# Kernel optimization log

Measured on AMD Instinct MI355X. Metric: run time of the kernel, lower is better.

The kernel has to match this reference:

```python
import jax, jax.numpy as jnp
import numpy as np

UNITS = 65
BATCH = 50
SEQ = 8192


def setup_inputs() -> dict:
    key = jax.random.key(0)
    ks = jax.random.split(key, 6)
    x = jax.random.normal(ks[0], (BATCH, SEQ, UNITS), dtype=jnp.float32)
    # Single shared LSTM cell (same cell object reused for all 3 stacked layers)
    W = jax.random.normal(ks[1], (UNITS, 4 * UNITS), dtype=jnp.float32) * 0.1
    U = jax.random.normal(ks[2], (UNITS, 4 * UNITS), dtype=jnp.float32) * 0.1
    b = jax.random.normal(ks[3], (4 * UNITS,), dtype=jnp.float32) * 0.1
    # Dense output projection 65 -> 65
    Wd = jax.random.normal(ks[4], (UNITS, UNITS), dtype=jnp.float32) * 0.1
    bd = jax.random.normal(ks[5], (UNITS,), dtype=jnp.float32) * 0.1
    return {"x": x, "W": W, "U": U, "b": b, "Wd": Wd, "bd": bd}


def _lstm_cell(x_t, h, c, W, U, b):
    # Keras LSTMCell: gates in order i, f, g(candidate), o
    z = x_t @ W + h @ U + b                      # [B, 4*units]
    i, f, g, o = jnp.split(z, 4, axis=-1)
    i = jax.nn.sigmoid(i)
    f = jax.nn.sigmoid(f)
    g = jnp.tanh(g)
    o = jax.nn.sigmoid(o)
    c_new = f * c + i * g
    h_new = o * jnp.tanh(c_new)
    return h_new, c_new


def reference(x, W, U, b, Wd, bd):
    B = x.shape[0]
    zeros = jnp.zeros((B, UNITS), dtype=x.dtype)
    init = (zeros, zeros, zeros, zeros, zeros, zeros)  # (h1,c1,h2,c2,h3,c3)

    def step(carry, x_t):
        h1, c1, h2, c2, h3, c3 = carry
        h1, c1 = _lstm_cell(x_t, h1, c1, W, U, b)  # layer 1 (shared weights)
        h2, c2 = _lstm_cell(h1, h2, c2, W, U, b)   # layer 2 (shared weights)
        h3, c3 = _lstm_cell(h2, h3, c3, W, U, b)   # layer 3 (shared weights)
        return (h1, c1, h2, c2, h3, c3), h3

    xs = jnp.swapaxes(x, 0, 1)                   # [T, B, 65]
    _, ys = jax.lax.scan(step, init, xs)         # ys: [T, B, 65]
    ys = jnp.swapaxes(ys, 0, 1)                  # [B, T, 65]
    out = ys @ Wd + bd                           # dense projection to vocab 65
    return out
```

## Files before the change

kernel.cpp:

```cpp
#include <hip/hip_runtime.h>

#define UNITS 65
#define SEQ   8192
#define BATCH 50
#define LAYER 192

typedef float v2f __attribute__((ext_vector_type(2)));

__device__ __forceinline__ float frcp(float x){ return __builtin_amdgcn_rcpf(x); }
__device__ __forceinline__ float fsigmoid(float x){ return frcp(1.0f + __expf(-x)); }
__device__ __forceinline__ float ftanh(float x){
    float e2 = __expf(2.0f * x);
    return 1.0f - 2.0f * frcp(e2 + 1.0f);
}

template<int CTRL>
__device__ __forceinline__ float dppadd(float x){
    int t = __builtin_amdgcn_update_dpp(0, __float_as_int(x), CTRL, 0xF, 0xF, true);
    return x + __int_as_float(t);
}
template<int CTRL>
__device__ __forceinline__ float dppmov(float x){
    int t = __builtin_amdgcn_update_dpp(0, __float_as_int(x), CTRL, 0xF, 0xF, true);
    return __int_as_float(t);
}
__device__ __forceinline__ float red4_all(float x){
    x = dppadd<0xB1>(x);
    x = dppadd<0x4E>(x);
    return x;
}
__device__ __forceinline__ float red16_lane15(float x){
    x = dppadd<0x111>(x);
    x = dppadd<0x112>(x);
    x = dppadd<0x114>(x);
    x = dppadd<0x118>(x);
    return x;
}
__device__ __forceinline__ void bar_lds(){
    asm volatile("s_waitcnt lgkmcnt(0)\n\ts_barrier" ::: "memory");
}
__device__ __forceinline__ float rdlane(float v, int l){
    return __int_as_float(__builtin_amdgcn_readlane(__float_as_int(v), l));
}

__device__ __forceinline__ int inpos16(int k){
    return (k < 120) ? ((k >> 3) * 12 + (k & 7)) : (180 + (k - 120));
}
__device__ __forceinline__ float wrow(const float* W, const float* U, int k, int c){
    return (k < 65) ? W[k * 260 + c] : U[(k - 65) * 260 + c];
}


#define LAYERB(aI, aF, aG, aO, CST, ...) do {                                  \
    float qI_ = red4_all(aI), qF_ = red4_all(aF);                              \
    float qG_ = red4_all(aG), qO_ = red4_all(aO);                              \
    float z_ = ((gsel == 0) ? qI_ : (gsel == 1) ? qF_ : (gsel == 2) ? qG_ : qO_); \
    z_ = dppadd<0x114>(z_);                        \
    z_ = dppadd<0x118>(z_);              \
    z_ += breg;                                                                \
    float sg_ = frcp(1.0f + __expf(-sk * z_));                                 \
    float g_  = fmaf(sk, sg_, dk);                \
    float gi_ = dppmov<0x113>(g_);                   \
    float gf_ = dppmov<0x112>(g_);                   \
    float gg_ = dppmov<0x111>(g_);                   \
    float cn_ = fmaf(gf_, CST, gi_ * gg_);                                     \
    float hn_ = g_ * ftanh(cn_);                                               \
    if (wr) { CST = cn_; __VA_ARGS__; }                                        \
} while (0)

#define STEP(L0, L1, L2, VB, NB) do {                                          \
    const float* __restrict__ vbase = (VB);                                    \
    float*       __restrict__ nbase = (NB);                                    \
          \
    float xq1 = 0.0f, ex1 = 0.0f;                                              \
    if (L0) {                                                                  \
        const int tl_ = (s + 2 < SEQ) ? (s + 2) : (SEQ - 1);                   \
        if (wr) xq1 = xrow[(size_t)tl_ * UNITS + j];                           \
        if (wave == 1 && lane == 0) ex1 = xrow[(size_t)tl_ * UNITS + 64];      \
    }                                                                          \
       \
    const float* vp0_ = vbase + k16 * 12;                                      \
    const float* vp1_ = vbase + LAYER + k16 * 12;                              \
    const float* vp2_ = vbase + 2 * LAYER + k16 * 12;                          \
    v2f aIF0={0,0},aGO0={0,0}, aIF1={0,0},aGO1={0,0}, aIF2={0,0},aGO2={0,0};   \
    _Pragma("unroll")                                                          \
    for (int q4_ = 0; q4_ < 2; ++q4_) {                                        \
        float4 f0_, f1_, f2_;                                                  \
        if (L0) f0_ = *(const float4*)(vp0_ + 4 * q4_);                        \
        if (L1) f1_ = *(const float4*)(vp1_ + 4 * q4_);                        \
        if (L2) f2_ = *(const float4*)(vp2_ + 4 * q4_);                        \
        _Pragma("unroll")                                                      \
        for (int r_ = 0; r_ < 4; ++r_) {                                       \
            const int kk = 4 * q4_ + r_;                                       \
            if (L0) { float s0_ = (&f0_.x)[r_]; v2f ss_ = {s0_, s0_};          \
                aIF0 = __builtin_elementwise_fma(ss_, wIF[kk], aIF0);          \
                aGO0 = __builtin_elementwise_fma(ss_, wGO[kk], aGO0); }        \
            if (L1) { float s1_ = (&f1_.x)[r_]; v2f ss_ = {s1_, s1_};          \
                aIF1 = __builtin_elementwise_fma(ss_, wIF[kk], aIF1);          \
                aGO1 = __builtin_elementwise_fma(ss_, wGO[kk], aGO1); }        \
            if (L2) { float s2_ = (&f2_.x)[r_]; v2f ss_ = {s2_, s2_};          \
                aIF2 = __builtin_elementwise_fma(ss_, wIF[kk], aIF2);          \
                aGO2 = __builtin_elementwise_fma(ss_, wGO[kk], aGO2); }        \
        }                                                                      \
    }                                                                          \
    {           \
        float2 t0_, t1_, t2_;                                                  \
        if (L0) t0_ = *(const float2*)(vp0_ + 8);                              \
        if (L1) t1_ = *(const float2*)(vp1_ + 8);                              \
        if (L2) t2_ = *(const float2*)(vp2_ + 8);                              \
        _Pragma("unroll")                                                      \
        for (int r_ = 0; r_ < 2; ++r_) {                                       \
            const int kk = 8 + r_;                                             \
            if (L0) { float s0_ = (&t0_.x)[r_]; v2f ss_ = {s0_, s0_};          \
                aIF0 = __builtin_elementwise_fma(ss_, wIF[kk], aIF0);          \
                aGO0 = __builtin_elementwise_fma(ss_, wGO[kk], aGO0); }        \
            if (L1) { float s1_ = (&t1_.x)[r_]; v2f ss_ = {s1_, s1_};          \
                aIF1 = __builtin_elementwise_fma(ss_, wIF[kk], aIF1);          \
                aGO1 = __builtin_elementwise_fma(ss_, wGO[kk], aGO1); }        \
            if (L2) { float s2_ = (&t2_.x)[r_]; v2f ss_ = {s2_, s2_};          \
                aIF2 = __builtin_elementwise_fma(ss_, wIF[kk], aIF2);          \
                aGO2 = __builtin_elementwise_fma(ss_, wGO[kk], aGO2); }        \
        }                                                                      \
    }                                                                          \
          \
    const bool act64_ = (wave == 1) ? (bool)(L0)                               \
                      : (wave == 2) ? (bool)(L1)                               \
                      : (wave == 3) ? (bool)(L2) : false;                      \
    float a64_ = 0.0f;                                                         \
    if (act64_) {                                                              \
        const float* vm_ = vbase + ml * LAYER;                                 \
        float4 uA_ = *(const float4*)(vm_ + p64);                              \
        float4 uB_ = *(const float4*)(vm_ + p64 + 4);                          \
        float  uex_ = (i64 < 2) ? vm_[188 + i64] : 0.0f;                       \
        a64_ = uA_.x * w64[0];                                                 \
        a64_ = fmaf(uA_.y, w64[1], a64_); a64_ = fmaf(uA_.z, w64[2], a64_);    \
        a64_ = fmaf(uA_.w, w64[3], a64_); a64_ = fmaf(uB_.x, w64[4], a64_);    \
        a64_ = fmaf(uB_.y, w64[5], a64_); a64_ = fmaf(uB_.z, w64[6], a64_);    \
        a64_ = fmaf(uB_.w, w64[7], a64_); a64_ = fmaf(uex_, w64x, a64_);       \
        a64_ = red16_lane15(a64_);                                             \
    }                                                                          \
                                            \
    if (L0) LAYERB(aIF0.x, aIF0.y, aGO0.x, aGO0.y, c1,                         \
                   nbase[ipH] = hn_; nbase[LAYER + ipI] = hn_);                \
    if (L1) LAYERB(aIF1.x, aIF1.y, aGO1.x, aGO1.y, c2,                         \
                   nbase[LAYER + ipH] = hn_; nbase[2 * LAYER + ipI] = hn_);    \
    if (L2) LAYERB(aIF2.x, aIF2.y, aGO2.x, aGO2.y, c3,                         \
                   nbase[2 * LAYER + ipH] = hn_;                               \
                   orow[(size_t)(s - 2) * UNITS + j] = hn_);                   \
    if (L0) { if (wr) { nbase[ipI] = xq0; xq0 = xq1; } }                       \
                               \
    if (act64_) {                                                              \
        float zi_ = rdlane(a64_, 15) + b64i;                                   \
        float zf_ = rdlane(a64_, 31) + b64f;                                   \
        float zg_ = rdlane(a64_, 47) + b64g;                                   \
        float zo_ = rdlane(a64_, 63) + b64o;                                   \
        float gi4_ = fsigmoid(zi_), gf4_ = fsigmoid(zf_);                      \
        float gg4_ = ftanh(zg_),    go4_ = fsigmoid(zo_);                      \
        float cn64_ = fmaf(gf4_, c64, gi4_ * gg4_);                            \
        float hn64_ = go4_ * ftanh(cn64_);                                     \
        c64 = cn64_;                                                           \
        if (lane == 0) {                                                       \
            nbase[ml * LAYER + 189] = hn64_;                     \
            if (wave <= 2) nbase[(ml + 1) * LAYER + 96] = hn64_;  \
            else orow[(size_t)(s - 2) * UNITS + 64] = hn64_;                   \
        }                                                                      \
        if (wave == 1) { if (lane == 0) nbase[96] = ex0; ex0 = ex1; }          \
    }                                                                          \
    bar_lds();                                                                 \
} while (0)

__global__ __launch_bounds__(1024, 4)
void lstm3_kernel(const float* __restrict__ x, const float* __restrict__ W,
                  const float* __restrict__ U, const float* __restrict__ b,
                  float* __restrict__ out)
{
    const int e    = blockIdx.x;
    const int tid  = threadIdx.x;
    const int wave = tid >> 6, lane = tid & 63;
    const int k16  = lane & 15, ul = lane >> 4;
    const int j    = wave * 4 + ul;
    const int gsel = k16 & 3;
    const bool wr  = (k16 == 15);

    __shared__ __attribute__((aligned(16))) float vbuf[2][3][LAYER];

    v2f wIF[10], wGO[10];
    #pragma unroll
    for (int kk = 0; kk < 10; ++kk) {
        const int  k   = 8 * k16 + kk;
        const bool val = (kk < 8) || (k16 == 15);
        wIF[kk].x = val ? wrow(W, U, k, j)       : 0.0f;
        wIF[kk].y = val ? wrow(W, U, k, 65  + j) : 0.0f;
        wGO[kk].x = val ? wrow(W, U, k, 130 + j) : 0.0f;
        wGO[kk].y = val ? wrow(W, U, k, 195 + j) : 0.0f;
    }
    const float breg = b[gsel * 65 + j];
    const float sk   = (gsel == 2) ? 2.0f : 1.0f;
    const float dk   = 1.0f - sk;

    const int i64 = lane & 15, g64 = lane >> 4;
    const int p64 = i64 * 12;
    float w64[8], w64x;
    {
        const int c64c = g64 * 65 + 64;
        #pragma unroll
        for (int r = 0; r < 8; ++r) w64[r] = wrow(W, U, 8 * i64 + r, c64c);
        w64x = (i64 < 2) ? wrow(W, U, 128 + i64, c64c) : 0.0f;
    }

    #pragma unroll
    for (int kk = 0; kk < 10; ++kk) {
        asm volatile("" : "+v"(wIF[kk]), "+v"(wGO[kk]));
    }
    #pragma unroll
    for (int r = 0; r < 8; ++r) { asm volatile("" : "+v"(w64[r])); }
    asm volatile("" : "+v"(w64x));

    const float b64i = b[64], b64f = b[129], b64g = b[194], b64o = b[259];
    const int ml = (wave >= 1 && wave <= 3) ? (wave - 1) : 0;

    float c1 = 0, c2 = 0, c3 = 0, c64 = 0;

    const float* xrow = x   + (size_t)e * SEQ * UNITS;
    float*       orow = out + (size_t)e * SEQ * UNITS;
    const int ipI = inpos16(j), ipH = inpos16(65 + j);

    for (int i = tid; i < 2 * 3 * LAYER; i += 1024) ((float*)&vbuf[0][0][0])[i] = 0.0f;
    __syncthreads();
    if (wr)  vbuf[0][0][ipI] = xrow[j];
    if (wave == 1 && lane == 0) vbuf[0][0][96] = xrow[64];
    __syncthreads();

    float xq0 = 0, ex0 = 0;
    if (wr) xq0 = xrow[UNITS + j];
    if (wave == 1 && lane == 0) ex0 = xrow[UNITS + 64];

    float* const vb0 = &vbuf[0][0][0];
    float* const vb1 = &vbuf[1][0][0];
    int s = 0;
    STEP(1, 0, 0, vb0, vb1); ++s;
    STEP(1, 1, 0, vb1, vb0); ++s;
    for (; s < SEQ - 1; ) {
        STEP(1, 1, 1, vb0, vb1); ++s;
        STEP(1, 1, 1, vb1, vb0); ++s;
    }
    STEP(0, 1, 1, vb0, vb1); ++s;
    STEP(0, 0, 1, vb1, vb0);
}

__global__ __launch_bounds__(256)
void dense_kernel(float* __restrict__ io,
                  const float* __restrict__ Wd,
                  const float* __restrict__ bd)
{
    __shared__ __attribute__((aligned(16))) float wS[65 * 68];
    __shared__ float bS[65];
    for (int i = threadIdx.x; i < 65 * 65; i += 256) {
        int r = i / 65, c = i - r * 65;
        wS[r * 68 + c] = Wd[i];
    }
    if (threadIdx.x < 65) bS[threadIdx.x] = bd[threadIdx.x];
    __syncthreads();

    const size_t row  = (size_t)blockIdx.x * 256 + threadIdx.x;
    const size_t base = row * 65;

    float r[65];
    #pragma unroll
    for (int k = 0; k < 65; ++k) r[k] = io[base + k];

    for (int ct = 0; ct < 16; ++ct) {
        const int c = ct * 4;
        float a0 = bS[c], a1 = bS[c + 1], a2 = bS[c + 2], a3 = bS[c + 3];
        #pragma unroll
        for (int k = 0; k < 65; ++k) {
            const float4 wv = *reinterpret_cast<const float4*>(&wS[k * 68 + c]);
            a0 += r[k] * wv.x;
            a1 += r[k] * wv.y;
            a2 += r[k] * wv.z;
            a3 += r[k] * wv.w;
        }
        io[base + c]     = a0;
        io[base + c + 1] = a1;
        io[base + c + 2] = a2;
        io[base + c + 3] = a3;
    }
    float a = bS[64];
    #pragma unroll
    for (int k = 0; k < 65; ++k) a += r[k] * wS[k * 68 + 64];
    io[base + 64] = a;
}

extern "C" void kernel_launch(void* const* d_in, const int* in_sizes, int n_in,
                              void* d_out, int out_size, void* d_ws, size_t ws_size,
                              hipStream_t stream)
{
    const float* x  = (const float*)d_in[0];
    const float* W  = (const float*)d_in[1];
    const float* U  = (const float*)d_in[2];
    const float* b  = (const float*)d_in[3];
    const float* Wd = (const float*)d_in[4];
    const float* bd = (const float*)d_in[5];
    float* out = (float*)d_out;

    hipLaunchKernelGGL(lstm3_kernel, dim3(BATCH), dim3(1024), 0, stream, x, W, U, b, out);
    hipLaunchKernelGGL(dense_kernel, dim3(1600), dim3(256), 0, stream, out, Wd, bd);
}
```

Measured before the change: 15.17 ms.

## Software-pipeline per-layer LDS reads, FMAs and gate math with wave-rotated layer order

Restructures each timestep so the three stacked layers are processed as a pipeline: it reads the next layer's LDS vector while finishing the FMAs and gate activations of the previous one. Each wave starts at a different layer (wave % 3), which spreads LDS bank traffic and SALU/transcendental work across waves. The unit-64 projection loads are hoisted ahead of the pipelined body, and the asm register pins on the weights are removed. Register pressure and code size grow because all three layer paths are instantiated per wave, and the three-way branch on wro adds control flow.

```diff
diff --git a/kernel.cpp b/kernel.cpp
--- a/kernel.cpp
+++ b/kernel.cpp
@@ -68,6 +68,53 @@
     if (wr) { CST = cn_; __VA_ARGS__; }                                        \
 } while (0)
 
+#define WRT_0  nbase[ipH] = hn_; nbase[LAYER + ipI] = hn_
+#define WRT_1  nbase[LAYER + ipH] = hn_; nbase[2 * LAYER + ipI] = hn_
+#define WRT_2  nbase[2 * LAYER + ipH] = hn_; orow[(size_t)(s - 2) * UNITS + j] = hn_
+
+#define RD(l, Lact) do { if (Lact) {                                           \
+    const float* vp_ = vbase + (l) * LAYER + k16 * 12;                         \
+    fA##l = *(const float4*)(vp_);                                             \
+    fB##l = *(const float4*)(vp_ + 4);                                         \
+    fT##l = *(const float2*)(vp_ + 8);                                         \
+} } while (0)
+
+#define FM(l, Lact) do { if (Lact) {                                           \
+    _Pragma("unroll")                                                          \
+    for (int r_ = 0; r_ < 4; ++r_) {                                           \
+        float s_ = (&fA##l.x)[r_]; v2f ss_ = {s_, s_};                         \
+        aIF##l = __builtin_elementwise_fma(ss_, wIF[r_], aIF##l);              \
+        aGO##l = __builtin_elementwise_fma(ss_, wGO[r_], aGO##l);              \
+    }                                                                          \
+    _Pragma("unroll")                                                          \
+    for (int r_ = 0; r_ < 4; ++r_) {                                           \
+        float s_ = (&fB##l.x)[r_]; v2f ss_ = {s_, s_};                         \
+        aIF##l = __builtin_elementwise_fma(ss_, wIF[4 + r_], aIF##l);          \
+        aGO##l = __builtin_elementwise_fma(ss_, wGO[4 + r_], aGO##l);          \
+    }                                                                          \
+    _Pragma("unroll")                                                          \
+    for (int r_ = 0; r_ < 2; ++r_) {                                           \
+        float s_ = (&fT##l.x)[r_]; v2f ss_ = {s_, s_};                         \
+        aIF##l = __builtin_elementwise_fma(ss_, wIF[8 + r_], aIF##l);          \
+        aGO##l = __builtin_elementwise_fma(ss_, wGO[8 + r_], aGO##l);          \
+    }                                                                          \
+} } while (0)
+
+#define PB0(Lact) do { if (Lact) LAYERB(aIF0.x, aIF0.y, aGO0.x, aGO0.y, c_0, WRT_0); } while (0)
+#define PB1(Lact) do { if (Lact) LAYERB(aIF1.x, aIF1.y, aGO1.x, aGO1.y, c_1, WRT_1); } while (0)
+#define PB2(Lact) do { if (Lact) LAYERB(aIF2.x, aIF2.y, aGO2.x, aGO2.y, c_2, WRT_2); } while (0)
+
+#define PIPE3(a, b, c, La, Lb, Lc) do {                                        \
+    RD(a, La); FM(a, La);                                                      \
+    RD(b, Lb);                                                                 \
+    PB##a(La);                                                                 \
+    FM(b, Lb);                                                                 \
+    RD(c, Lc);                                                                 \
+    PB##b(Lb);                                                                 \
+    FM(c, Lc);                                                                 \
+    PB##c(Lc);                                                                 \
+} while (0)
+
 #define STEP(L0, L1, L2, VB, NB) do {                                          \
     const float* __restrict__ vbase = (VB);                                    \
     float*       __restrict__ nbase = (NB);                                    \
@@ -79,77 +126,31 @@
         if (wave == 1 && lane == 0) ex1 = xrow[(size_t)tl_ * UNITS + 64];      \
     }                                                                          \
        \
-    const float* vp0_ = vbase + k16 * 12;                                      \
-    const float* vp1_ = vbase + LAYER + k16 * 12;                              \
-    const float* vp2_ = vbase + 2 * LAYER + k16 * 12;                          \
-    v2f aIF0={0,0},aGO0={0,0}, aIF1={0,0},aGO1={0,0}, aIF2={0,0},aGO2={0,0};   \
-    _Pragma("unroll")                                                          \
-    for (int q4_ = 0; q4_ < 2; ++q4_) {                                        \
-        float4 f0_, f1_, f2_;                                                  \
-        if (L0) f0_ = *(const float4*)(vp0_ + 4 * q4_);                        \
-        if (L1) f1_ = *(const float4*)(vp1_ + 4 * q4_);                        \
-        if (L2) f2_ = *(const float4*)(vp2_ + 4 * q4_);                        \
-        _Pragma("unroll")                                                      \
-        for (int r_ = 0; r_ < 4; ++r_) {                                       \
-            const int kk = 4 * q4_ + r_;                                       \
-            if (L0) { float s0_ = (&f0_.x)[r_]; v2f ss_ = {s0_, s0_};          \
-                aIF0 = __builtin_elementwise_fma(ss_, wIF[kk], aIF0);          \
-                aGO0 = __builtin_elementwise_fma(ss_, wGO[kk], aGO0); }        \
-            if (L1) { float s1_ = (&f1_.x)[r_]; v2f ss_ = {s1_, s1_};          \
-                aIF1 = __builtin_elementwise_fma(ss_, wIF[kk], aIF1);          \
-                aGO1 = __builtin_elementwise_fma(ss_, wGO[kk], aGO1); }        \
-            if (L2) { float s2_ = (&f2_.x)[r_]; v2f ss_ = {s2_, s2_};          \
-                aIF2 = __builtin_elementwise_fma(ss_, wIF[kk], aIF2);          \
-                aGO2 = __builtin_elementwise_fma(ss_, wGO[kk], aGO2); }        \
-        }                                                                      \
-    }                                                                          \
-    {           \
-        float2 t0_, t1_, t2_;                                                  \
-        if (L0) t0_ = *(const float2*)(vp0_ + 8);                              \
-        if (L1) t1_ = *(const float2*)(vp1_ + 8);                              \
-        if (L2) t2_ = *(const float2*)(vp2_ + 8);                              \
-        _Pragma("unroll")                                                      \
-        for (int r_ = 0; r_ < 2; ++r_) {                                       \
-            const int kk = 8 + r_;                                             \
-            if (L0) { float s0_ = (&t0_.x)[r_]; v2f ss_ = {s0_, s0_};          \
-                aIF0 = __builtin_elementwise_fma(ss_, wIF[kk], aIF0);          \
-                aGO0 = __builtin_elementwise_fma(ss_, wGO[kk], aGO0); }        \
-            if (L1) { float s1_ = (&t1_.x)[r_]; v2f ss_ = {s1_, s1_};          \
-                aIF1 = __builtin_elementwise_fma(ss_, wIF[kk], aIF1);          \
-                aGO1 = __builtin_elementwise_fma(ss_, wGO[kk], aGO1); }        \
-            if (L2) { float s2_ = (&t2_.x)[r_]; v2f ss_ = {s2_, s2_};          \
-                aIF2 = __builtin_elementwise_fma(ss_, wIF[kk], aIF2);          \
-                aGO2 = __builtin_elementwise_fma(ss_, wGO[kk], aGO2); }        \
-        }                                                                      \
-    }                                                                          \
-          \
     const bool act64_ = (wave == 1) ? (bool)(L0)                               \
                       : (wave == 2) ? (bool)(L1)                               \
                       : (wave == 3) ? (bool)(L2) : false;                      \
-    float a64_ = 0.0f;                                                         \
+    float4 uA_ = {0,0,0,0}, uB_ = {0,0,0,0}; float uex_ = 0.0f;                \
     if (act64_) {                                                              \
         const float* vm_ = vbase + ml * LAYER;                                 \
-        float4 uA_ = *(const float4*)(vm_ + p64);                              \
-        float4 uB_ = *(const float4*)(vm_ + p64 + 4);                          \
-        float  uex_ = (i64 < 2) ? vm_[188 + i64] : 0.0f;                       \
-        a64_ = uA_.x * w64[0];                                                 \
+        uA_ = *(const float4*)(vm_ + p64);                                     \
+        uB_ = *(const float4*)(vm_ + p64 + 4);                                 \
+        uex_ = (i64 < 2) ? vm_[188 + i64] : 0.0f;                              \
+    }                                                                          \
+    float4 fA0, fB0, fA1, fB1, fA2, fB2; float2 fT0, fT1, fT2;                 \
+    v2f aIF0={0,0},aGO0={0,0}, aIF1={0,0},aGO1={0,0}, aIF2={0,0},aGO2={0,0};   \
+           \
+    if (wro == 0)      PIPE3(0, 1, 2, L0, L1, L2);                             \
+    else if (wro == 1) PIPE3(1, 2, 0, L1, L2, L0);                             \
+    else               PIPE3(2, 0, 1, L2, L0, L1);                             \
+    if (L0) { if (wr) { nbase[ipI] = xq0; xq0 = xq1; } }                       \
+                 \
+    if (act64_) {                                                              \
+        float a64_ = uA_.x * w64[0];                                           \
         a64_ = fmaf(uA_.y, w64[1], a64_); a64_ = fmaf(uA_.z, w64[2], a64_);    \
         a64_ = fmaf(uA_.w, w64[3], a64_); a64_ = fmaf(uB_.x, w64[4], a64_);    \
         a64_ = fmaf(uB_.y, w64[5], a64_); a64_ = fmaf(uB_.z, w64[6], a64_);    \
         a64_ = fmaf(uB_.w, w64[7], a64_); a64_ = fmaf(uex_, w64x, a64_);       \
         a64_ = red16_lane15(a64_);                                             \
-    }                                                                          \
-                                            \
-    if (L0) LAYERB(aIF0.x, aIF0.y, aGO0.x, aGO0.y, c1,                         \
-                   nbase[ipH] = hn_; nbase[LAYER + ipI] = hn_);                \
-    if (L1) LAYERB(aIF1.x, aIF1.y, aGO1.x, aGO1.y, c2,                         \
-                   nbase[LAYER + ipH] = hn_; nbase[2 * LAYER + ipI] = hn_);    \
-    if (L2) LAYERB(aIF2.x, aIF2.y, aGO2.x, aGO2.y, c3,                         \
-                   nbase[2 * LAYER + ipH] = hn_;                               \
-                   orow[(size_t)(s - 2) * UNITS + j] = hn_);                   \
-    if (L0) { if (wr) { nbase[ipI] = xq0; xq0 = xq1; } }                       \
-                               \
-    if (act64_) {                                                              \
         float zi_ = rdlane(a64_, 15) + b64i;                                   \
         float zf_ = rdlane(a64_, 31) + b64f;                                   \
         float zg_ = rdlane(a64_, 47) + b64g;                                   \
@@ -181,6 +182,7 @@
     const int j    = wave * 4 + ul;
     const int gsel = k16 & 3;
     const bool wr  = (k16 == 15);
+    const int wro  = wave % 3;
 
     __shared__ __attribute__((aligned(16))) float vbuf[2][3][LAYER];
 
@@ -207,19 +209,10 @@
         for (int r = 0; r < 8; ++r) w64[r] = wrow(W, U, 8 * i64 + r, c64c);
         w64x = (i64 < 2) ? wrow(W, U, 128 + i64, c64c) : 0.0f;
     }
-
-    #pragma unroll
-    for (int kk = 0; kk < 10; ++kk) {
-        asm volatile("" : "+v"(wIF[kk]), "+v"(wGO[kk]));
-    }
-    #pragma unroll
-    for (int r = 0; r < 8; ++r) { asm volatile("" : "+v"(w64[r])); }
-    asm volatile("" : "+v"(w64x));
-
     const float b64i = b[64], b64f = b[129], b64g = b[194], b64o = b[259];
     const int ml = (wave >= 1 && wave <= 3) ? (wave - 1) : 0;
 
-    float c1 = 0, c2 = 0, c3 = 0, c64 = 0;
+    float c_0 = 0, c_1 = 0, c_2 = 0, c64 = 0;
 
     const float* xrow = x   + (size_t)e * SEQ * UNITS;
     float*       orow = out + (size_t)e * SEQ * UNITS;
```

Result: no change. 15.06 ms (-0.7%).
